# Performance work log

Hardware: AMD Instinct MI355X
Metric: run time of the kernel (lower is better)

The kernel has to match this reference:

```python
import jax, jax.numpy as jnp
import numpy as np

D = 2        # dof (input_dim of fc1)
H1 = 64      # hidden width
N = 262144   # batch
NEG_SLOPE = -0.01  # NOTE: original uses self.neg_slope=-0.01 in the analytic derivative
                   # while the forward activation uses F.leaky_relu default slope +0.01.
                   # We replicate this exactly.

def _lin_init(k, out_d, in_d):
    bound = 1.0 / np.sqrt(in_d)
    kw, kb = jax.random.split(k)
    W = jax.random.uniform(kw, (out_d, in_d), minval=-bound, maxval=bound, dtype=jnp.float32)
    b = jax.random.uniform(kb, (out_d,), minval=-bound, maxval=bound, dtype=jnp.float32)
    return W, b

def setup_inputs():
    key = jax.random.key(0)
    ks = jax.random.split(key, 6)
    W1, b1 = _lin_init(ks[0], H1, D)
    W1a, b1a = _lin_init(ks[1], H1, H1)
    W2, b2 = _lin_init(ks[2], D, H1)
    W3, b3 = _lin_init(ks[3], D, H1)
    W4, b4 = _lin_init(ks[4], 1, H1)
    x = jax.random.normal(ks[5], (N, 3 * D), dtype=jnp.float32)
    return {"x": x, "W1": W1, "b1": b1, "W1a": W1a, "b1a": b1a,
            "W2": W2, "b2": b2, "W3": W3, "b3": b3, "W4": W4, "b4": b4}

def _forward(x, W1, b1, W1a, b1a, W2, b2, W3, b3, W4, b4):
    n = x.shape[0]
    d = x.shape[1] // 3
    q, qd, qdd = x[:, :d], x[:, d:2 * d], x[:, 2 * d:]

    h1 = jax.nn.leaky_relu(q @ W1.T + b1, 0.01)       # [n,H1]
    h2 = jax.nn.leaky_relu(h1 @ W1a.T + b1a, 0.01)    # [n,H1]
    g = h2 @ W2.T + b2                                # [n,d]
    ld = jax.nn.relu(h2 @ W3.T + b3)                  # [n,d]  diagonal of L
    lo = h2 @ W4.T + b4                               # [n,1]  off-diagonal(s)

    # Analytic Jacobians. diag_embed(a) @ W == a[:,:,None] * W (no [n,H,H] materialization).
    dR1 = jnp.where(h1 > 0, 1.0, NEG_SLOPE)
    dh1_dq = dR1[:, :, None] * W1[None]                              # [n,H1,d]
    dR2 = jnp.where(h2 > 0, 1.0, NEG_SLOPE)
    dh2_dq = dR2[:, :, None] * jnp.einsum('hk,nkd->nhd', W1a, dh1_dq)  # [n,H1,d]
    dR3 = jnp.where(ld > 0, 1.0, 0.0)
    dld_dq = dR3[:, :, None] * jnp.einsum('oh,nhd->nod', W3, dh2_dq)   # [n,d,d]
    dlo_dq = jnp.einsum('oh,nhd->nod', W4, dh2_dq)                     # [n,1,d]

    dld_dqi = jnp.transpose(dld_dq, (0, 2, 1))[..., None]  # [n,d,d,1]
    dlo_dqi = jnp.transpose(dlo_dq, (0, 2, 1))[..., None]  # [n,d,1,1]
    dld_dt = dld_dq @ qd[:, :, None]                       # [n,d,1]
    dlo_dt = dlo_dq @ qd[:, :, None]                       # [n,1,1]

    zeros = jnp.zeros_like(ld)
    zeros2 = jnp.zeros_like(dld_dqi)
    Lc, dLt, dLq = [], [], []
    s, e = 0, d - 1
    for i in range(d):  # loop over d (=2) columns of the Cholesky factor
        Lc.append(jnp.concatenate([zeros[:, :i], ld[:, i:i + 1], lo[:, s:e]], axis=1))
        dLt.append(jnp.concatenate([zeros[:, :i], dld_dt[:, i].reshape(n, 1),
                                    dlo_dt[:, s:e].reshape(n, -1)], axis=1))
        dLq.append(jnp.concatenate([zeros2[:, :, :i].reshape(n, d, -1),
                                    dld_dqi[:, :, i].reshape(n, d, 1),
                                    dlo_dqi[:, :, s:e].reshape(n, d, -1)], axis=2))
        s, e = s + e, e + d - 2 - i
    L = jnp.stack(Lc, axis=2)                                    # [n,d,d]
    dL_dt = jnp.stack(dLt, axis=2)                               # [n,d,d]
    dL_dqi = jnp.transpose(jnp.stack(dLq, axis=3), (0, 2, 3, 1)) # [n,d,d,d]

    eps = 1e-5
    Lt = jnp.swapaxes(L, 1, 2)
    Hm = L @ Lt + eps * jnp.eye(d, dtype=x.dtype)
    dH_dt = L @ jnp.swapaxes(dL_dt, 1, 2) + dL_dt @ Lt

    qts = []
    for i in range(d):
        A = dL_dqi[..., i] @ Lt + L @ jnp.swapaxes(dL_dqi[..., i], 1, 2)
        qts.append(qd[:, None, :] @ A @ qd[:, :, None])  # [n,1,1]
    quad = jnp.stack(qts, axis=1).reshape(n, d, 1)

    c = dH_dt @ qd[:, :, None] - 0.5 * quad
    tau = Hm @ qdd[:, :, None] + c + g[:, :, None]
    return tau[..., 0], Hm, c[..., 0], g

def reference(x, W1, b1, W1a, b1a, W2, b2, W3, b3, W4, b4):
    return _forward(x, W1, b1, W1a, b1a, W2, b2, W3, b3, W4, b4)
```

## Files before the change

kernel.cpp:

```cpp
#include <hip/hip_runtime.h>
#include <stdint.h>


typedef __attribute__((ext_vector_type(8))) _Float16 f16x8;
typedef __attribute__((ext_vector_type(4))) float f32x4;
typedef __attribute__((ext_vector_type(2))) float f32x2;
typedef __attribute__((ext_vector_type(4))) unsigned int u32x4;

#define MFMA16(A,B,C) __builtin_amdgcn_mfma_f32_16x16x32_f16((A),(B),(C),0,0,0)

static __device__ __forceinline__ f32x2 pk_fma(f32x2 a, f32x2 b, f32x2 c) {
    f32x2 d;
    asm("v_pk_fma_f32 %0, %1, %2, %3" : "=v"(d) : "v"(a), "v"(b), "v"(c));
    return d;
}
static __device__ __forceinline__ f32x2 pk_mul(f32x2 a, f32x2 b) {
    f32x2 d;
    asm("v_pk_mul_f32 %0, %1, %2" : "=v"(d) : "v"(a), "v"(b));
    return d;
}
static __device__ __forceinline__ unsigned pkmul16(unsigned a, unsigned b) {
    unsigned d;
    asm("v_pk_mul_f16 %0, %1, %2" : "=v"(d) : "v"(a), "v"(b));
    return d;
}
static __device__ __forceinline__ float qsum(float v) {
    float a = v, b = v;
    asm("v_permlane16_swap_b32 %0, %1" : "+v"(a), "+v"(b));
    const float s = a + b;
    float c = s, d = s;
    asm("v_permlane32_swap_b32 %0, %1" : "+v"(c), "+v"(d));
    return c + d;
}

__global__ __launch_bounds__(256, 4) void delan_fwd(
    const float* __restrict__ x,
    const float* __restrict__ W1,  const float* __restrict__ b1,
    const float* __restrict__ W1a, const float* __restrict__ b1a,
    const float* __restrict__ W2,  const float* __restrict__ b2,
    const float* __restrict__ W3,  const float* __restrict__ b3,
    const float* __restrict__ W4,  const float* __restrict__ b4,
    float* __restrict__ out, int n_total)
{
    __shared__ _Float16 afrag[2][4][2][64][8];
    __shared__ float w0s[64], w1s[64], bs[64];
    __shared__ float cst[6][64];

    const int tid  = threadIdx.x;
    const int lane = tid & 63;
    const int wid  = tid >> 6;
    const int p    = lane & 15;
    const int qrt  = lane >> 4;
    const int n    = blockIdx.x * 256 + tid;
    const int nc   = (n < n_total) ? n : (n_total - 1);

    const float2 xa = *(const float2*)(x + 6 * nc);
    const float2 xb = *(const float2*)(x + 6 * nc + 2);
    const float2 xc = *(const float2*)(x + 6 * nc + 4);
    const float x0 = xa.x, x1 = xa.y;
    const float x2 = xb.x, x3 = xb.y;
    const float x4 = xc.x, x5 = xc.y;

    if (tid < 64) {
        const int k = tid;
        w0s[k] = W1[2*k]; w1s[k] = W1[2*k+1]; bs[k] = b1[k];
        cst[0][k] = W2[k];      cst[1][k] = W2[64 + k];
        cst[2][k] = W3[k];      cst[3][k] = W3[64 + k];
        cst[4][k] = W4[k];      cst[5][k] = b1a[k];
    }
    {
        const int ht = wid;
#pragma unroll
        for (int kh = 0; kh < 2; ++kh) {
            const int row = ht * 16 + p;
            const int kb  = kh * 32 + qrt * 8;
            float wv[8];
            *(float4*)&wv[0] = *(const float4*)(W1a + row * 64 + kb);
            *(float4*)&wv[4] = *(const float4*)(W1a + row * 64 + kb + 4);
            f16x8 hi, lo;
#pragma unroll
            for (int j = 0; j < 8; ++j) {
                const _Float16 h = (_Float16)wv[j];
                hi[j] = h;
                lo[j] = (_Float16)((wv[j] - (float)h) * 4096.0f);
            }
            *(f16x8*)&afrag[0][ht][kh][lane][0] = hi;
            *(f16x8*)&afrag[1][ht][kh][lane][0] = lo;
        }
    }
    __syncthreads();

    const f32x2 c4096  = {4096.0f, 4096.0f};
    const f32x2 cm4096 = {-4096.0f, -4096.0f};

    float fg0=0.f, fg1=0.f, fl0=0.f, fl1=0.f, foo=0.f;
    float fp00=0.f, fp01=0.f, fp10=0.f, fp11=0.f, fr0=0.f, fr1=0.f;

#pragma unroll
    for (int t = 0; t < 4; ++t) {
        const float q0t = __shfl(x0, t * 16 + p);
        const float q1t = __shfl(x1, t * 16 + p);
        const f32x2 q00 = {q0t, q0t};
        const f32x2 q11 = {q1t, q1t};
        u32x4 Bhh[2], Bhl[2], Bu0[2], Bu1[2];
#pragma unroll
        for (int kh = 0; kh < 2; ++kh) {
            const int kb = kh * 32 + qrt * 8;
#pragma unroll
            for (int c = 0; c < 4; ++c) {
                const f32x2 w0p = *(const f32x2*)&w0s[kb + 2*c];
                const f32x2 w1p = *(const f32x2*)&w1s[kb + 2*c];
                const f32x2 bp  = *(const f32x2*)&bs [kb + 2*c];
                const f32x2 prep = pk_fma(w0p, q00, pk_fma(w1p, q11, bp));
                const bool pos0 = prep.x > 0.0f;
                const bool pos1 = prep.y > 0.0f;
                const unsigned mlo = pos0 ? 0x00003C00u : 0x0000A11Fu;
                const unsigned mhi = pos1 ? 0x3C000000u : 0xA11F0000u;
                const unsigned drw = mlo | mhi;
                const unsigned p0w = __builtin_bit_cast(unsigned,
                    __builtin_amdgcn_cvt_pkrtz(w0p.x, w0p.y));
                const unsigned p1w = __builtin_bit_cast(unsigned,
                    __builtin_amdgcn_cvt_pkrtz(w1p.x, w1p.y));
                Bu0[kh][c] = pkmul16(p0w, drw);
                Bu1[kh][c] = pkmul16(p1w, drw);
                f32x2 sp;
                sp.x = pos0 ? 1.0f : 0.01f;
                sp.y = pos1 ? 1.0f : 0.01f;
                const f32x2 h1p = pk_mul(prep, sp);
                const auto hhv = __builtin_amdgcn_cvt_pkrtz(h1p.x, h1p.y);
                Bhh[kh][c] = __builtin_bit_cast(unsigned, hhv);
                f32x2 hf;
                hf.x = (float)hhv[0];
                hf.y = (float)hhv[1];
                const f32x2 tt = pk_mul(h1p, c4096);
                const f32x2 rp = pk_fma(hf, cm4096, tt);
                Bhl[kh][c] = __builtin_bit_cast(unsigned,
                    __builtin_amdgcn_cvt_pkrtz(rp.x, rp.y));
            }
        }

        float ag0=0.f, ag1=0.f, al0=0.f, al1=0.f, aoo=0.f;
        float ap00=0.f, ap01=0.f, ap10=0.f, ap11=0.f, ar0=0.f, ar1=0.f;
#pragma unroll
        for (int ht = 0; ht < 4; ++ht) {
            const f16x8 Ah0 = *(const f16x8*)&afrag[0][ht][0][lane][0];
            const f16x8 Ah1 = *(const f16x8*)&afrag[0][ht][1][lane][0];
            const f16x8 Al0 = *(const f16x8*)&afrag[1][ht][0][lane][0];
            const f16x8 Al1 = *(const f16x8*)&afrag[1][ht][1][lane][0];
            const f16x8 bh0 = __builtin_bit_cast(f16x8, Bhh[0]);
            const f16x8 bh1 = __builtin_bit_cast(f16x8, Bhh[1]);
            const f16x8 bl0 = __builtin_bit_cast(f16x8, Bhl[0]);
            const f16x8 bl1 = __builtin_bit_cast(f16x8, Bhl[1]);
            const f16x8 bu00 = __builtin_bit_cast(f16x8, Bu0[0]);
            const f16x8 bu01 = __builtin_bit_cast(f16x8, Bu0[1]);
            const f16x8 bu10 = __builtin_bit_cast(f16x8, Bu1[0]);
            const f16x8 bu11 = __builtin_bit_cast(f16x8, Bu1[1]);

            const int hb = ht * 16 + qrt * 4;
            f32x4 Chi = *(const f32x4*)&cst[5][hb];
            f32x4 Clo = {0.f,0.f,0.f,0.f};
            f32x4 Cz0 = {0.f,0.f,0.f,0.f};
            f32x4 Cz1 = {0.f,0.f,0.f,0.f};
            Chi = MFMA16(Ah0, bh0, Chi);  Chi = MFMA16(Ah1, bh1, Chi);
            Clo = MFMA16(Ah0, bl0, Clo);  Clo = MFMA16(Ah1, bl1, Clo);
            Clo = MFMA16(Al0, bh0, Clo);  Clo = MFMA16(Al1, bh1, Clo);
            Cz0 = MFMA16(Ah0, bu00, Cz0); Cz0 = MFMA16(Ah1, bu01, Cz0);
            Cz1 = MFMA16(Ah0, bu10, Cz1); Cz1 = MFMA16(Ah1, bu11, Cz1);

            const f32x4 w2a  = *(const f32x4*)&cst[0][hb];
            const f32x4 w2b  = *(const f32x4*)&cst[1][hb];
            const f32x4 w3a  = *(const f32x4*)&cst[2][hb];
            const f32x4 w3b  = *(const f32x4*)&cst[3][hb];
            const f32x4 w4v  = *(const f32x4*)&cst[4][hb];
#pragma unroll
            for (int r = 0; r < 4; ++r) {
                const float ah = fmaf(2.44140625e-4f, Clo[r], Chi[r]);
                const bool pos = ah > 0.0f;
                const float h2 = pos ? ah : 0.01f * ah;
                ag0 = fmaf(w2a[r], h2, ag0);   ag1 = fmaf(w2b[r], h2, ag1);
                al0 = fmaf(w3a[r], h2, al0);   al1 = fmaf(w3b[r], h2, al1);
                aoo = fmaf(w4v[r], h2, aoo);
                const float z0 = Cz0[r], z1 = Cz1[r];
                const float d0 = pos ? z0 : -0.01f * z0;
                const float d1 = pos ? z1 : -0.01f * z1;
                ap00 = fmaf(w3a[r], d0, ap00); ap01 = fmaf(w3a[r], d1, ap01);
                ap10 = fmaf(w3b[r], d0, ap10); ap11 = fmaf(w3b[r], d1, ap11);
                ar0  = fmaf(w4v[r], d0, ar0);  ar1  = fmaf(w4v[r], d1, ar1);
            }
        }

        ag0 = qsum(ag0); ag1 = qsum(ag1); al0 = qsum(al0); al1 = qsum(al1);
        aoo = qsum(aoo);
        ap00 = qsum(ap00); ap01 = qsum(ap01); ap10 = qsum(ap10); ap11 = qsum(ap11);
        ar0 = qsum(ar0);  ar1 = qsum(ar1);
        if (qrt == t) {
            fg0 = ag0; fg1 = ag1; fl0 = al0; fl1 = al1; foo = aoo;
            fp00 = ap00; fp01 = ap01; fp10 = ap10; fp11 = ap11;
            fr0 = ar0; fr1 = ar1;
        }
    }

    const float g0 = fg0 + b2[0], g1 = fg1 + b2[1];
    const float l0 = fl0 + b3[0], l1 = fl1 + b3[1];
    const float oo = foo + b4[0];
    const float p00 = fp00, p01 = fp01, p10 = fp10, p11 = fp11;
    const float r0 = fr0, r1 = fr1;

    const float ld0 = fmaxf(l0, 0.0f);
    const float ld1 = fmaxf(l1, 0.0f);
    const float dr30 = (l0 > 0.0f) ? 1.0f : 0.0f;
    const float dr31 = (l1 > 0.0f) ? 1.0f : 0.0f;

    const float da00 = dr30 * p00, da01 = dr30 * p01;
    const float da10 = dr31 * p10, da11 = dr31 * p11;

    const float l00 = ld0, l10 = oo, l11 = ld1;

    const float m00 = da00 * x2 + da01 * x3;
    const float m11 = da10 * x2 + da11 * x3;
    const float m10 = r0  * x2 + r1  * x3;

    const float eps = 1e-5f;
    const float Hm00 = fmaf(l00, l00, eps);
    const float Hm01 = l00 * l10;
    const float Hm11 = fmaf(l10, l10, fmaf(l11, l11, eps));

    const float dH00 = 2.0f * l00 * m00;
    const float dH01 = fmaf(l00, m10, l10 * m00);
    const float dH11 = 2.0f * fmaf(l10, m10, l11 * m11);

    const float x22 = x2 * x2, x23 = x2 * x3, x33 = x3 * x3;
    const float quad0 = 2.0f * (da00 * l00 * x22
                      + (fmaf(da00, l10, r0 * l00)) * x23
                      + (fmaf(r0, l10, da10 * l11)) * x33);
    const float quad1 = 2.0f * (da01 * l00 * x22
                      + (fmaf(da01, l10, r1 * l00)) * x23
                      + (fmaf(r1, l10, da11 * l11)) * x33);

    const float c0 = fmaf(dH00, x2, dH01 * x3) - 0.5f * quad0;
    const float c1 = fmaf(dH01, x2, dH11 * x3) - 0.5f * quad1;

    const float tau0 = fmaf(Hm00, x4, Hm01 * x5) + c0 + g0;
    const float tau1 = fmaf(Hm01, x4, Hm11 * x5) + c1 + g1;

    if (n < n_total) {
        const long long N = n_total;
        float2* tau_out = (float2*)(out) + n;
        float4* hm_out  = (float4*)(out + 2 * N) + n;
        float2* c_out   = (float2*)(out + 6 * N) + n;
        float2* g_out   = (float2*)(out + 8 * N) + n;
        *tau_out = make_float2(tau0, tau1);
        *hm_out  = make_float4(Hm00, Hm01, Hm01, Hm11);
        *c_out   = make_float2(c0, c1);
        *g_out   = make_float2(g0, g1);
    }
}

extern "C" void kernel_launch(void* const* d_in, const int* in_sizes, int n_in,
                              void* d_out, int out_size, void* d_ws, size_t ws_size,
                              hipStream_t stream) {
    const float* x   = (const float*)d_in[0];
    const float* W1  = (const float*)d_in[1];
    const float* b1  = (const float*)d_in[2];
    const float* W1a = (const float*)d_in[3];
    const float* b1a = (const float*)d_in[4];
    const float* W2  = (const float*)d_in[5];
    const float* b2  = (const float*)d_in[6];
    const float* W3  = (const float*)d_in[7];
    const float* b3  = (const float*)d_in[8];
    const float* W4  = (const float*)d_in[9];
    const float* b4  = (const float*)d_in[10];
    float* out = (float*)d_out;

    const int n_total = in_sizes[0] / 6;
    const int block = 256;
    const int grid = (n_total + block - 1) / block;
    delan_fwd<<<grid, block, 0, stream>>>(x, W1, b1, W1a, b1a, W2, b2,
                                          W3, b3, W4, b4, out, n_total);
}
```

Before: 30.31 us.

## Map one sample per 16-lane group to drop the per-wave four-tile loop

```diff
diff --git a/kernel.cpp b/kernel.cpp
--- a/kernel.cpp
+++ b/kernel.cpp
@@ -51,12 +51,12 @@
     const int wid  = tid >> 6;
     const int p    = lane & 15;
     const int qrt  = lane >> 4;
-    const int n    = blockIdx.x * 256 + tid;
-    const int nc   = (n < n_total) ? n : (n_total - 1);
-
-    const float2 xa = *(const float2*)(x + 6 * nc);
-    const float2 xb = *(const float2*)(x + 6 * nc + 2);
-    const float2 xc = *(const float2*)(x + 6 * nc + 4);
+    const int s    = blockIdx.x * 64 + wid * 16 + p;
+    const int sc   = (s < n_total) ? s : (n_total - 1);
+
+    const float2 xa = *(const float2*)(x + 6 * sc);
+    const float2 xb = *(const float2*)(x + 6 * sc + 2);
+    const float2 xc = *(const float2*)(x + 6 * sc + 4);
     const float x0 = xa.x, x1 = xa.y;
     const float x2 = xb.x, x3 = xb.y;
     const float x4 = xc.x, x5 = xc.y;
@@ -93,118 +93,103 @@
     const f32x2 c4096  = {4096.0f, 4096.0f};
     const f32x2 cm4096 = {-4096.0f, -4096.0f};
 
-    float fg0=0.f, fg1=0.f, fl0=0.f, fl1=0.f, foo=0.f;
-    float fp00=0.f, fp01=0.f, fp10=0.f, fp11=0.f, fr0=0.f, fr1=0.f;
-
-#pragma unroll
-    for (int t = 0; t < 4; ++t) {
-        const float q0t = __shfl(x0, t * 16 + p);
-        const float q1t = __shfl(x1, t * 16 + p);
-        const f32x2 q00 = {q0t, q0t};
-        const f32x2 q11 = {q1t, q1t};
-        u32x4 Bhh[2], Bhl[2], Bu0[2], Bu1[2];
-#pragma unroll
-        for (int kh = 0; kh < 2; ++kh) {
-            const int kb = kh * 32 + qrt * 8;
-#pragma unroll
-            for (int c = 0; c < 4; ++c) {
-                const f32x2 w0p = *(const f32x2*)&w0s[kb + 2*c];
-                const f32x2 w1p = *(const f32x2*)&w1s[kb + 2*c];
-                const f32x2 bp  = *(const f32x2*)&bs [kb + 2*c];
-                const f32x2 prep = pk_fma(w0p, q00, pk_fma(w1p, q11, bp));
-                const bool pos0 = prep.x > 0.0f;
-                const bool pos1 = prep.y > 0.0f;
-                const unsigned mlo = pos0 ? 0x00003C00u : 0x0000A11Fu;
-                const unsigned mhi = pos1 ? 0x3C000000u : 0xA11F0000u;
-                const unsigned drw = mlo | mhi;
-                const unsigned p0w = __builtin_bit_cast(unsigned,
-                    __builtin_amdgcn_cvt_pkrtz(w0p.x, w0p.y));
-                const unsigned p1w = __builtin_bit_cast(unsigned,
-                    __builtin_amdgcn_cvt_pkrtz(w1p.x, w1p.y));
-                Bu0[kh][c] = pkmul16(p0w, drw);
-                Bu1[kh][c] = pkmul16(p1w, drw);
-                f32x2 sp;
-                sp.x = pos0 ? 1.0f : 0.01f;
-                sp.y = pos1 ? 1.0f : 0.01f;
-                const f32x2 h1p = pk_mul(prep, sp);
-                const auto hhv = __builtin_amdgcn_cvt_pkrtz(h1p.x, h1p.y);
-                Bhh[kh][c] = __builtin_bit_cast(unsigned, hhv);
-                f32x2 hf;
-                hf.x = (float)hhv[0];
-                hf.y = (float)hhv[1];
-                const f32x2 tt = pk_mul(h1p, c4096);
-                const f32x2 rp = pk_fma(hf, cm4096, tt);
-                Bhl[kh][c] = __builtin_bit_cast(unsigned,
-                    __builtin_amdgcn_cvt_pkrtz(rp.x, rp.y));
-            }
-        }
-
-        float ag0=0.f, ag1=0.f, al0=0.f, al1=0.f, aoo=0.f;
-        float ap00=0.f, ap01=0.f, ap10=0.f, ap11=0.f, ar0=0.f, ar1=0.f;
-#pragma unroll
-        for (int ht = 0; ht < 4; ++ht) {
-            const f16x8 Ah0 = *(const f16x8*)&afrag[0][ht][0][lane][0];
-            const f16x8 Ah1 = *(const f16x8*)&afrag[0][ht][1][lane][0];
-            const f16x8 Al0 = *(const f16x8*)&afrag[1][ht][0][lane][0];
-            const f16x8 Al1 = *(const f16x8*)&afrag[1][ht][1][lane][0];
-            const f16x8 bh0 = __builtin_bit_cast(f16x8, Bhh[0]);
-            const f16x8 bh1 = __builtin_bit_cast(f16x8, Bhh[1]);
-            const f16x8 bl0 = __builtin_bit_cast(f16x8, Bhl[0]);
-            const f16x8 bl1 = __builtin_bit_cast(f16x8, Bhl[1]);
-            const f16x8 bu00 = __builtin_bit_cast(f16x8, Bu0[0]);
-            const f16x8 bu01 = __builtin_bit_cast(f16x8, Bu0[1]);
-            const f16x8 bu10 = __builtin_bit_cast(f16x8, Bu1[0]);
-            const f16x8 bu11 = __builtin_bit_cast(f16x8, Bu1[1]);
-
-            const int hb = ht * 16 + qrt * 4;
-            f32x4 Chi = *(const f32x4*)&cst[5][hb];
-            f32x4 Clo = {0.f,0.f,0.f,0.f};
-            f32x4 Cz0 = {0.f,0.f,0.f,0.f};
-            f32x4 Cz1 = {0.f,0.f,0.f,0.f};
-            Chi = MFMA16(Ah0, bh0, Chi);  Chi = MFMA16(Ah1, bh1, Chi);
-            Clo = MFMA16(Ah0, bl0, Clo);  Clo = MFMA16(Ah1, bl1, Clo);
-            Clo = MFMA16(Al0, bh0, Clo);  Clo = MFMA16(Al1, bh1, Clo);
-            Cz0 = MFMA16(Ah0, bu00, Cz0); Cz0 = MFMA16(Ah1, bu01, Cz0);
-            Cz1 = MFMA16(Ah0, bu10, Cz1); Cz1 = MFMA16(Ah1, bu11, Cz1);
-
-            const f32x4 w2a  = *(const f32x4*)&cst[0][hb];
-            const f32x4 w2b  = *(const f32x4*)&cst[1][hb];
-            const f32x4 w3a  = *(const f32x4*)&cst[2][hb];
-            const f32x4 w3b  = *(const f32x4*)&cst[3][hb];
-            const f32x4 w4v  = *(const f32x4*)&cst[4][hb];
-#pragma unroll
-            for (int r = 0; r < 4; ++r) {
-                const float ah = fmaf(2.44140625e-4f, Clo[r], Chi[r]);
-                const bool pos = ah > 0.0f;
-                const float h2 = pos ? ah : 0.01f * ah;
-                ag0 = fmaf(w2a[r], h2, ag0);   ag1 = fmaf(w2b[r], h2, ag1);
-                al0 = fmaf(w3a[r], h2, al0);   al1 = fmaf(w3b[r], h2, al1);
-                aoo = fmaf(w4v[r], h2, aoo);
-                const float z0 = Cz0[r], z1 = Cz1[r];
-                const float d0 = pos ? z0 : -0.01f * z0;
-                const float d1 = pos ? z1 : -0.01f * z1;
-                ap00 = fmaf(w3a[r], d0, ap00); ap01 = fmaf(w3a[r], d1, ap01);
-                ap10 = fmaf(w3b[r], d0, ap10); ap11 = fmaf(w3b[r], d1, ap11);
-                ar0  = fmaf(w4v[r], d0, ar0);  ar1  = fmaf(w4v[r], d1, ar1);
-            }
-        }
-
-        ag0 = qsum(ag0); ag1 = qsum(ag1); al0 = qsum(al0); al1 = qsum(al1);
-        aoo = qsum(aoo);
-        ap00 = qsum(ap00); ap01 = qsum(ap01); ap10 = qsum(ap10); ap11 = qsum(ap11);
-        ar0 = qsum(ar0);  ar1 = qsum(ar1);
-        if (qrt == t) {
-            fg0 = ag0; fg1 = ag1; fl0 = al0; fl1 = al1; foo = aoo;
-            fp00 = ap00; fp01 = ap01; fp10 = ap10; fp11 = ap11;
-            fr0 = ar0; fr1 = ar1;
-        }
-    }
-
-    const float g0 = fg0 + b2[0], g1 = fg1 + b2[1];
-    const float l0 = fl0 + b3[0], l1 = fl1 + b3[1];
-    const float oo = foo + b4[0];
-    const float p00 = fp00, p01 = fp01, p10 = fp10, p11 = fp11;
-    const float r0 = fr0, r1 = fr1;
+    const f32x2 q00 = {x0, x0};
+    const f32x2 q11 = {x1, x1};
+    u32x4 Bhh[2], Bhl[2], Bu0[2], Bu1[2];
+#pragma unroll
+    for (int kh = 0; kh < 2; ++kh) {
+        const int kb = kh * 32 + qrt * 8;
+#pragma unroll
+        for (int c = 0; c < 4; ++c) {
+            const f32x2 w0p = *(const f32x2*)&w0s[kb + 2*c];
+            const f32x2 w1p = *(const f32x2*)&w1s[kb + 2*c];
+            const f32x2 bp  = *(const f32x2*)&bs [kb + 2*c];
+            const f32x2 prep = pk_fma(w0p, q00, pk_fma(w1p, q11, bp));
+            const bool pos0 = prep.x > 0.0f;
+            const bool pos1 = prep.y > 0.0f;
+            const unsigned mlo = pos0 ? 0x00003C00u : 0x0000A11Fu;
+            const unsigned mhi = pos1 ? 0x3C000000u : 0xA11F0000u;
+            const unsigned drw = mlo | mhi;
+            const unsigned p0w = __builtin_bit_cast(unsigned,
+                __builtin_amdgcn_cvt_pkrtz(w0p.x, w0p.y));
+            const unsigned p1w = __builtin_bit_cast(unsigned,
+                __builtin_amdgcn_cvt_pkrtz(w1p.x, w1p.y));
+            Bu0[kh][c] = pkmul16(p0w, drw);
+            Bu1[kh][c] = pkmul16(p1w, drw);
+            f32x2 sp;
+            sp.x = pos0 ? 1.0f : 0.01f;
+            sp.y = pos1 ? 1.0f : 0.01f;
+            const f32x2 h1p = pk_mul(prep, sp);
+            const auto hhv = __builtin_amdgcn_cvt_pkrtz(h1p.x, h1p.y);
+            Bhh[kh][c] = __builtin_bit_cast(unsigned, hhv);
+            f32x2 hf;
+            hf.x = (float)hhv[0];
+            hf.y = (float)hhv[1];
+            const f32x2 tt = pk_mul(h1p, c4096);
+            const f32x2 rp = pk_fma(hf, cm4096, tt);
+            Bhl[kh][c] = __builtin_bit_cast(unsigned,
+                __builtin_amdgcn_cvt_pkrtz(rp.x, rp.y));
+        }
+    }
+
+    float ag0=0.f, ag1=0.f, al0=0.f, al1=0.f, aoo=0.f;
+    float ap00=0.f, ap01=0.f, ap10=0.f, ap11=0.f, ar0=0.f, ar1=0.f;
+#pragma unroll
+    for (int ht = 0; ht < 4; ++ht) {
+        const f16x8 Ah0 = *(const f16x8*)&afrag[0][ht][0][lane][0];
+        const f16x8 Ah1 = *(const f16x8*)&afrag[0][ht][1][lane][0];
+        const f16x8 Al0 = *(const f16x8*)&afrag[1][ht][0][lane][0];
+        const f16x8 Al1 = *(const f16x8*)&afrag[1][ht][1][lane][0];
+        const f16x8 bh0 = __builtin_bit_cast(f16x8, Bhh[0]);
+        const f16x8 bh1 = __builtin_bit_cast(f16x8, Bhh[1]);
+        const f16x8 bl0 = __builtin_bit_cast(f16x8, Bhl[0]);
+        const f16x8 bl1 = __builtin_bit_cast(f16x8, Bhl[1]);
+        const f16x8 bu00 = __builtin_bit_cast(f16x8, Bu0[0]);
+        const f16x8 bu01 = __builtin_bit_cast(f16x8, Bu0[1]);
+        const f16x8 bu10 = __builtin_bit_cast(f16x8, Bu1[0]);
+        const f16x8 bu11 = __builtin_bit_cast(f16x8, Bu1[1]);
+
+        const int hb = ht * 16 + qrt * 4;
+        f32x4 Chi = *(const f32x4*)&cst[5][hb];
+        f32x4 Clo = {0.f,0.f,0.f,0.f};
+        f32x4 Cz0 = {0.f,0.f,0.f,0.f};
+        f32x4 Cz1 = {0.f,0.f,0.f,0.f};
+        Chi = MFMA16(Ah0, bh0, Chi);  Chi = MFMA16(Ah1, bh1, Chi);
+        Clo = MFMA16(Ah0, bl0, Clo);  Clo = MFMA16(Ah1, bl1, Clo);
+        Clo = MFMA16(Al0, bh0, Clo);  Clo = MFMA16(Al1, bh1, Clo);
+        Cz0 = MFMA16(Ah0, bu00, Cz0); Cz0 = MFMA16(Ah1, bu01, Cz0);
+        Cz1 = MFMA16(Ah0, bu10, Cz1); Cz1 = MFMA16(Ah1, bu11, Cz1);
+
+        const f32x4 w2a  = *(const f32x4*)&cst[0][hb];
+        const f32x4 w2b  = *(const f32x4*)&cst[1][hb];
+        const f32x4 w3a  = *(const f32x4*)&cst[2][hb];
+        const f32x4 w3b  = *(const f32x4*)&cst[3][hb];
+        const f32x4 w4v  = *(const f32x4*)&cst[4][hb];
+#pragma unroll
+        for (int r = 0; r < 4; ++r) {
+            const float ah = fmaf(2.44140625e-4f, Clo[r], Chi[r]);
+            const bool pos = ah > 0.0f;
+            const float h2 = pos ? ah : 0.01f * ah;
+            ag0 = fmaf(w2a[r], h2, ag0);   ag1 = fmaf(w2b[r], h2, ag1);
+            al0 = fmaf(w3a[r], h2, al0);   al1 = fmaf(w3b[r], h2, al1);
+            aoo = fmaf(w4v[r], h2, aoo);
+            const float z0 = Cz0[r], z1 = Cz1[r];
+            const float d0 = pos ? z0 : -0.01f * z0;
+            const float d1 = pos ? z1 : -0.01f * z1;
+            ap00 = fmaf(w3a[r], d0, ap00); ap01 = fmaf(w3a[r], d1, ap01);
+            ap10 = fmaf(w3b[r], d0, ap10); ap11 = fmaf(w3b[r], d1, ap11);
+            ar0  = fmaf(w4v[r], d0, ar0);  ar1  = fmaf(w4v[r], d1, ar1);
+        }
+    }
+
+    const float g0 = qsum(ag0) + b2[0];
+    const float g1 = qsum(ag1) + b2[1];
+    const float l0 = qsum(al0) + b3[0];
+    const float l1 = qsum(al1) + b3[1];
+    const float oo = qsum(aoo) + b4[0];
+    const float p00 = qsum(ap00), p01 = qsum(ap01);
+    const float p10 = qsum(ap10), p11 = qsum(ap11);
+    const float r0 = qsum(ar0),  r1 = qsum(ar1);
 
     const float ld0 = fmaxf(l0, 0.0f);
     const float ld1 = fmaxf(l1, 0.0f);
@@ -243,16 +228,17 @@
     const float tau0 = fmaf(Hm00, x4, Hm01 * x5) + c0 + g0;
     const float tau1 = fmaf(Hm01, x4, Hm11 * x5) + c1 + g1;
 
-    if (n < n_total) {
+    if (s < n_total) {
         const long long N = n_total;
-        float2* tau_out = (float2*)(out) + n;
-        float4* hm_out  = (float4*)(out + 2 * N) + n;
-        float2* c_out   = (float2*)(out + 6 * N) + n;
-        float2* g_out   = (float2*)(out + 8 * N) + n;
-        *tau_out = make_float2(tau0, tau1);
-        *hm_out  = make_float4(Hm00, Hm01, Hm01, Hm11);
-        *c_out   = make_float2(c0, c1);
-        *g_out   = make_float2(g0, g1);
+        if (qrt == 0) {
+            *((float2*)out + s) = make_float2(tau0, tau1);
+        } else if (qrt == 1) {
+            *((float4*)(out + 2 * N) + s) = make_float4(Hm00, Hm01, Hm01, Hm11);
+        } else if (qrt == 2) {
+            *((float2*)(out + 6 * N) + s) = make_float2(c0, c1);
+        } else {
+            *((float2*)(out + 8 * N) + s) = make_float2(g0, g1);
+        }
     }
 }
 
@@ -274,7 +260,7 @@
 
     const int n_total = in_sizes[0] / 6;
     const int block = 256;
-    const int grid = (n_total + block - 1) / block;
+    const int grid = (n_total + 63) / 64;
     delan_fwd<<<grid, block, 0, stream>>>(x, W1, b1, W1a, b1a, W2, b2,
                                           W3, b3, W4, b4, out, n_total);
 }
```

After: 30.60 us. No clear change (+0.9%).
